# Performance work log

Measured on AMD Instinct MI355X. Metric: run time of the kernel, lower is better.

## Reference

```python
import jax, jax.numpy as jnp
import numpy as np

TOP_K = 2  # num_experts_per_token


def setup_inputs() -> dict:
    key = jax.random.key(0)
    ks = jax.random.split(key, 6)
    B, S, H, F, E = 4, 2048, 1024, 4096, 8  # F = 2 * intermediate_size
    scale = 0.02
    x = jax.random.normal(ks[0], (B, S, H), dtype=jnp.float32)
    gate_w = jax.random.normal(ks[1], (E, H), dtype=jnp.float32) * scale
    w1 = jax.random.normal(ks[2], (E, H, F), dtype=jnp.float32) * scale
    b1 = jnp.zeros((E, F), dtype=jnp.float32)
    w2 = jax.random.normal(ks[3], (E, F, H), dtype=jnp.float32) * scale
    b2 = jnp.zeros((E, H), dtype=jnp.float32)
    return {"x": x, "gate_w": gate_w, "w1": w1, "b1": b1, "w2": w2, "b2": b2}


def reference(x, gate_w, w1, b1, w2, b2):
    # x: [B, S, H]; gate_w: [E, H]; w1: [E, H, F]; b1: [E, F]; w2: [E, F, H]; b2: [E, H]
    E = gate_w.shape[0]
    gate_logits = jnp.einsum('bsh,eh->bse', x, gate_w)
    gate_probs = jax.nn.softmax(gate_logits, axis=-1)
    top_v, top_i = jax.lax.top_k(gate_probs, TOP_K)  # [B, S, K]
    # Combine weight per expert: w[b,s,e] = sum_k top_v[b,s,k] * (top_i[b,s,k] == e)
    onehot = jax.nn.one_hot(top_i, E, dtype=x.dtype)          # [B, S, K, E]
    comb_w = jnp.einsum('bsk,bske->bse', top_v, onehot)       # [B, S, E]
    out = jnp.zeros_like(x)
    for e in range(E):  # small fixed expert loop
        h = jax.nn.silu(jnp.einsum('bsh,hf->bsf', x, w1[e]) + b1[e])
        y = jnp.einsum('bsf,fh->bsh', h, w2[e]) + b2[e]
        out = out + y * comb_w[..., e:e + 1]
    return out
```

## Files before the change

kernel.cpp:

```cpp
#include <hip/hip_runtime.h>
#include <stdint.h>

#define T_TOK 8192
#define HDIM  1024
#define FDIM  4096
#define NEXP  8
#define BT    256
#define RCAP  (2*T_TOK + NEXP*256)
#define LDSB  65536

typedef short  short8  __attribute__((ext_vector_type(8)));
typedef unsigned short ushort8 __attribute__((ext_vector_type(8)));
typedef float  f32x4   __attribute__((ext_vector_type(4)));

#define MFMA __builtin_amdgcn_mfma_f32_16x16x32_bf16

__device__ __forceinline__ unsigned short f2bf(float f) {
  unsigned u = __float_as_uint(f);
  u += 0x7fffu + ((u >> 16) & 1u);
  return (unsigned short)(u >> 16);
}
__device__ __forceinline__ float bf2f(unsigned short u) {
  return __uint_as_float((unsigned)u << 16);
}

__device__ __forceinline__ void gload16(const void* g, void* l) {
  __builtin_amdgcn_global_load_lds(
      (const __attribute__((address_space(1))) void*)g,
      (__attribute__((address_space(3))) void*)l, 16, 0, 0);
}

__global__ __launch_bounds__(256) void k_transp_cvt(const float* __restrict__ in,
                                                    unsigned short* __restrict__ out,
                                                    int K, int N) {
  __shared__ unsigned short s[64][72];
  const float* ine = in + (size_t)blockIdx.z * K * N;
  unsigned short* oute = out + (size_t)blockIdx.z * K * N;
  int k0 = blockIdx.y * 64, n0 = blockIdx.x * 64;
  int t = threadIdx.x;
  int kr = t >> 4, nc = (t & 15) * 4;
#pragma unroll
  for (int it = 0; it < 4; ++it) {
    int k = it * 16 + kr;
    float4 v = *(const float4*)(ine + (size_t)(k0 + k) * N + n0 + nc);
    ushort4 u = make_ushort4(f2bf(v.x), f2bf(v.y), f2bf(v.z), f2bf(v.w));
    *(ushort4*)(&s[k][nc]) = u;
  }
  __syncthreads();
  int nr = t >> 3, kc = (t & 7) * 8;
#pragma unroll
  for (int v = 0; v < 2; ++v) {
    int n = v * 32 + nr;
    ushort8 o;
#pragma unroll
    for (int j = 0; j < 8; ++j) o[j] = s[kc + j][n];
    *(ushort8*)(oute + (size_t)(n0 + n) * K + k0 + kc) = o;
  }
}

__global__ void k_gate(const float* __restrict__ x, const float* __restrict__ gw,
                       unsigned short* __restrict__ xb,
                       int2* __restrict__ eidx, float2* __restrict__ ewt) {
  int tid = threadIdx.x;
  int lane = tid & 63;
  int t = blockIdx.x * 4 + (tid >> 6);
  const float* xr = x + (size_t)t * HDIM;
  unsigned short* xbr = xb + (size_t)t * HDIM;
  float acc[NEXP];
#pragma unroll
  for (int e = 0; e < NEXP; e++) acc[e] = 0.f;
#pragma unroll
  for (int i = 0; i < HDIM / 64; i++) {
    float xv = xr[i * 64 + lane];
    xbr[i * 64 + lane] = f2bf(xv);
#pragma unroll
    for (int e = 0; e < NEXP; e++) acc[e] += xv * gw[e * HDIM + i * 64 + lane];
  }
#pragma unroll
  for (int e = 0; e < NEXP; e++) {
    acc[e] += __shfl_xor(acc[e], 32);
    acc[e] += __shfl_xor(acc[e], 16);
    acc[e] += __shfl_xor(acc[e], 8);
    acc[e] += __shfl_xor(acc[e], 4);
    acc[e] += __shfl_xor(acc[e], 2);
    acc[e] += __shfl_xor(acc[e], 1);
  }
  float m = acc[0];
#pragma unroll
  for (int e = 1; e < NEXP; e++) m = fmaxf(m, acc[e]);
  float p[NEXP]; float s = 0.f;
#pragma unroll
  for (int e = 0; e < NEXP; e++) { p[e] = expf(acc[e] - m); s += p[e]; }
  float inv = 1.f / s;
#pragma unroll
  for (int e = 0; e < NEXP; e++) p[e] *= inv;
  int b0 = 0; float v0 = p[0];
#pragma unroll
  for (int e = 1; e < NEXP; e++) if (p[e] > v0) { v0 = p[e]; b0 = e; }
  int b1i = (b0 == 0) ? 1 : 0; float v1 = p[b1i];
#pragma unroll
  for (int e = 0; e < NEXP; e++) if (e != b0 && p[e] > v1) { v1 = p[e]; b1i = e; }
  if (lane == 0) { eidx[t] = make_int2(b0, b1i); ewt[t] = make_float2(v0, v1); }
}

__global__ void k_compact(const int2* __restrict__ eidx,
                          int* __restrict__ list_tok, int* __restrict__ counts) {
  int e = blockIdx.x;
  int tid = threadIdx.x, lane = tid & 63, wid = tid >> 6;
  __shared__ int sbase;
  __shared__ int wcnt[4];
  if (tid == 0) sbase = 0;
  __syncthreads();
  for (int c = 0; c < T_TOK; c += 256) {
    int t = c + tid;
    int2 ei = eidx[t];
    bool sel = (ei.x == e) || (ei.y == e);
    unsigned long long b = __ballot(sel);
    if (lane == 0) wcnt[wid] = __popcll(b);
    __syncthreads();
    int pre = sbase;
    for (int w = 0; w < wid; w++) pre += wcnt[w];
    int pos = pre + __popcll(b & ((1ull << lane) - 1ull));
    if (sel) list_tok[e * T_TOK + pos] = t;
    __syncthreads();
    if (tid == 0) sbase += wcnt[0] + wcnt[1] + wcnt[2] + wcnt[3];
    __syncthreads();
  }
  if (tid == 0) counts[e] = sbase;
}

__global__ void k_offsets(const int* __restrict__ counts, int* __restrict__ off_pad) {
  if (threadIdx.x == 0) {
    int o = 0;
    off_pad[0] = 0;
    for (int e = 0; e < NEXP; e++) {
      o += ((counts[e] + BT - 1) / BT) * BT;
      off_pad[e + 1] = o;
    }
  }
}

__global__ void k_invert(const int* __restrict__ list_tok, const int* __restrict__ counts,
                         const int* __restrict__ off_pad, const int2* __restrict__ eidx,
                         int2* __restrict__ tok2slot) {
  int e = blockIdx.y;
  int p = blockIdx.x * 256 + threadIdx.x;
  if (p < counts[e]) {
    int t = list_tok[e * T_TOK + p];
    int slot = off_pad[e] + p;
    if (eidx[t].x == e) tok2slot[t].x = slot;
    else                tok2slot[t].y = slot;
  }
}

#define STAGE_A(u_, v_) { \
    char* lb_ = smem + (((v_)&1) ? LDSB : 0) + (u_)*16384; \
    gload16(gA[u_][0] + (size_t)(v_)*128, lb_ + dst0); \
    gload16(gA[u_][1] + (size_t)(v_)*128, lb_ + dst1); }
#define STAGE_B(u_, v_) { \
    char* lb_ = smem + (((v_)&1) ? LDSB : 0) + 32768 + (u_)*16384; \
    gload16(gB[u_][0] + (size_t)(v_)*128, lb_ + dst0); \
    gload16(gB[u_][1] + (size_t)(v_)*128, lb_ + dst1); }

#define PHASE(MA, MB, STAGE_STMT, TAIL_STMT) { \
    short8 aA0 = *(const short8*)(pA0 + (MA)*2048); \
    short8 aA1 = *(const short8*)(pA1 + (MA)*2048); \
    short8 aB0 = *(const short8*)(pA0 + (MB)*2048); \
    short8 aB1 = *(const short8*)(pA1 + (MB)*2048); \
    STAGE_STMT; \
    __builtin_amdgcn_s_barrier(); \
    asm volatile("s_waitcnt lgkmcnt(0)" ::: "memory"); \
    __builtin_amdgcn_sched_barrier(0); \
    __builtin_amdgcn_s_setprio(1); \
    acc[MA][0] = MFMA(aA0, b00, acc[MA][0], 0,0,0); acc[MA][0] = MFMA(aA1, b01, acc[MA][0], 0,0,0); \
    acc[MA][1] = MFMA(aA0, b10, acc[MA][1], 0,0,0); acc[MA][1] = MFMA(aA1, b11, acc[MA][1], 0,0,0); \
    acc[MA][2] = MFMA(aA0, b20, acc[MA][2], 0,0,0); acc[MA][2] = MFMA(aA1, b21, acc[MA][2], 0,0,0); \
    acc[MA][3] = MFMA(aA0, b30, acc[MA][3], 0,0,0); acc[MA][3] = MFMA(aA1, b31, acc[MA][3], 0,0,0); \
    acc[MB][0] = MFMA(aB0, b00, acc[MB][0], 0,0,0); acc[MB][0] = MFMA(aB1, b01, acc[MB][0], 0,0,0); \
    acc[MB][1] = MFMA(aB0, b10, acc[MB][1], 0,0,0); acc[MB][1] = MFMA(aB1, b11, acc[MB][1], 0,0,0); \
    acc[MB][2] = MFMA(aB0, b20, acc[MB][2], 0,0,0); acc[MB][2] = MFMA(aB1, b21, acc[MB][2], 0,0,0); \
    acc[MB][3] = MFMA(aB0, b30, acc[MB][3], 0,0,0); acc[MB][3] = MFMA(aB1, b31, acc[MB][3], 0,0,0); \
    __builtin_amdgcn_s_setprio(0); \
    TAIL_STMT; \
    __builtin_amdgcn_s_barrier(); }

#define READ_B4 \
    short8 b00 = *(const short8*)(pB0),        b01 = *(const short8*)(pB1); \
    short8 b10 = *(const short8*)(pB0 + 2048), b11 = *(const short8*)(pB1 + 2048); \
    short8 b20 = *(const short8*)(pB0 + 4096), b21 = *(const short8*)(pB1 + 4096); \
    short8 b30 = *(const short8*)(pB0 + 6144), b31 = *(const short8*)(pB1 + 6144);

#define GEMM_TILE_LOOP(NT) \
  STAGE_A(0,0); STAGE_A(1,0); STAGE_B(0,0); STAGE_B(1,0); STAGE_B(0,1); STAGE_B(1,1); \
  asm volatile("s_waitcnt vmcnt(4)" ::: "memory"); \
  __builtin_amdgcn_s_barrier(); \
  for (int v = 0; v < (NT); ++v) { \
    const char* bufb = smem + ((v&1) ? LDSB : 0); \
    const char* pA0 = bufb + wm * 16384 + aoff0; \
    const char* pA1 = bufb + wm * 16384 + aoff1; \
    const char* pB0 = bufb + 32768 + (wn >> 1) * 16384 + boff0; \
    const char* pB1 = bufb + 32768 + (wn >> 1) * 16384 + boff1; \
    READ_B4; \
    PHASE(0, 1, { if (v+1 < (NT)) STAGE_A(0, v+1); }, {}); \
    PHASE(2, 3, { if (v+1 < (NT)) STAGE_A(1, v+1); }, {}); \
    PHASE(4, 5, { if (v+2 < (NT)) STAGE_B(0, v+2); }, {}); \
    PHASE(6, 7, { if (v+2 < (NT)) STAGE_B(1, v+2); }, { \
      if (v+2 < (NT))      { asm volatile("s_waitcnt vmcnt(4)" ::: "memory"); } \
      else if (v+1 < (NT)) { asm volatile("s_waitcnt vmcnt(0)" ::: "memory"); } }); \
  }

__global__ __launch_bounds__(512, 2) void k_gemm1(
    const unsigned short* __restrict__ xb, const unsigned short* __restrict__ w1t,
    const float* __restrict__ b1, const int* __restrict__ list_tok,
    const int* __restrict__ counts, const int* __restrict__ off_pad,
    unsigned short* __restrict__ h) {
  extern __shared__ char smem[];
  int wl = (blockIdx.x & 7) * 144 + (blockIdx.x >> 3);
  int r0 = (wl >> 4) * BT;
  int n0 = (wl & 15) * BT;
  if (r0 >= off_pad[NEXP]) return;
  int e = 0;
#pragma unroll
  for (int i = 0; i < NEXP; ++i) if (r0 >= off_pad[i + 1]) e = i + 1;
  int base = off_pad[e], cnt = counts[e];

  int t = threadIdx.x, l = t & 63, w = t >> 6;
  int wm = w >> 2, wn = w & 3;
  int lr = l & 15, g16 = (l >> 4) * 16;
  int swz = (lr & 7) << 4;
  int aoff0 = lr * 128 + (g16 ^ swz);
  int aoff1 = lr * 128 + ((64 + g16) ^ swz);
  int boff0 = (wn & 1) * 8192 + aoff0;
  int boff1 = (wn & 1) * 8192 + aoff1;

  int dst0 = t * 16, dst1 = t * 16 + 8192;
  int srow = t >> 3;
  int skb = (((t & 7) ^ ((t >> 3) & 7)) << 4);
  const char* gA[2][2];
  const char* gB[2][2];
#pragma unroll
  for (int u = 0; u < 2; ++u)
#pragma unroll
    for (int j = 0; j < 2; ++j) {
      int row = u * 128 + srow + 64 * j;
      int se = r0 - base + row;
      int tok = (se < cnt) ? list_tok[e * T_TOK + se] : 0;
      gA[u][j] = (const char*)(xb + (size_t)tok * HDIM) + skb;
      gB[u][j] = (const char*)(w1t + (size_t)e * FDIM * HDIM + (size_t)(n0 + row) * HDIM) + skb;
    }

  f32x4 acc[8][4];
#pragma unroll
  for (int m = 0; m < 8; ++m)
#pragma unroll
    for (int n = 0; n < 4; ++n) acc[m][n] = (f32x4){0.f, 0.f, 0.f, 0.f};

  GEMM_TILE_LOOP(HDIM / 64);

  const float* b1e = b1 + (size_t)e * FDIM + n0;
  unsigned short* Cs = (unsigned short*)smem;
  int lh = l >> 4, lh4 = lh * 4;
  int cswz = lh << 4;
#pragma unroll
  for (int n = 0; n < 4; ++n) {
    int col = wn * 64 + n * 16 + lr;
    int colX = col ^ cswz;
    float bv = b1e[col];
#pragma unroll
    for (int m = 0; m < 8; ++m) {
      int row = wm * 128 + m * 16 + lh4;
#pragma unroll
      for (int i = 0; i < 4; ++i) {
        float vv = acc[m][n][i] + bv;
        float sg = __builtin_amdgcn_rcpf(1.f + __expf(-vv));
        Cs[(size_t)(row + i) * BT + colX] = f2bf(vv * sg);
      }
    }
  }
  __syncthreads();
#pragma unroll
  for (int s = 0; s < 16; ++s) {
    int lin = s * 512 + t;
    int row = lin >> 5, c8 = (lin & 31) * 8;
    int c8X = c8 ^ (((row >> 2) & 3) << 4);
    *(ushort8*)(h + (size_t)(r0 + row) * FDIM + n0 + c8) = *(const ushort8*)(Cs + (size_t)row * BT + c8X);
  }
}

__global__ __launch_bounds__(512, 2) void k_gemm2(
    const unsigned short* __restrict__ h, const unsigned short* __restrict__ w2t,
    const float* __restrict__ b2, const int* __restrict__ off_pad,
    unsigned short* __restrict__ ypartA, unsigned short* __restrict__ ypartB) {
  extern __shared__ char smem[];
  int wl = (blockIdx.x & 7) * 72 + (blockIdx.x >> 3);
  int mB = wl >> 3, rem = wl & 7;
  int r0 = mB * BT;
  int n0 = (rem >> 1) * BT;
  int z  = rem & 1;
  if (r0 >= off_pad[NEXP]) return;
  int e = 0;
#pragma unroll
  for (int i = 0; i < NEXP; ++i) if (r0 >= off_pad[i + 1]) e = i + 1;

  int t = threadIdx.x, l = t & 63, w = t >> 6;
  int wm = w >> 2, wn = w & 3;
  int lr = l & 15, g16 = (l >> 4) * 16;
  int swz = (lr & 7) << 4;
  int aoff0 = lr * 128 + (g16 ^ swz);
  int aoff1 = lr * 128 + ((64 + g16) ^ swz);
  int boff0 = (wn & 1) * 8192 + aoff0;
  int boff1 = (wn & 1) * 8192 + aoff1;

  int dst0 = t * 16, dst1 = t * 16 + 8192;
  int srow = t >> 3;
  int skb = (((t & 7) ^ ((t >> 3) & 7)) << 4);
  const char* gA[2][2];
  const char* gB[2][2];
#pragma unroll
  for (int u = 0; u < 2; ++u)
#pragma unroll
    for (int j = 0; j < 2; ++j) {
      int row = u * 128 + srow + 64 * j;
      gA[u][j] = (const char*)(h + (size_t)(r0 + row) * FDIM + (size_t)z * 2048) + skb;
      gB[u][j] = (const char*)(w2t + (size_t)e * HDIM * FDIM + (size_t)(n0 + row) * FDIM + (size_t)z * 2048) + skb;
    }

  f32x4 acc[8][4];
#pragma unroll
  for (int m = 0; m < 8; ++m)
#pragma unroll
    for (int n = 0; n < 4; ++n) acc[m][n] = (f32x4){0.f, 0.f, 0.f, 0.f};

  GEMM_TILE_LOOP(2048 / 64);

  const float* b2e = b2 + (size_t)e * HDIM + n0;
  unsigned short* yp = z ? ypartB : ypartA;
  unsigned short* Cs = (unsigned short*)smem;
  int lh = l >> 4, lh4 = lh * 4;
  int cswz = lh << 4;
#pragma unroll
  for (int n = 0; n < 4; ++n) {
    int col = wn * 64 + n * 16 + lr;
    int colX = col ^ cswz;
    float bv = (z == 0) ? b2e[col] : 0.f;
#pragma unroll
    for (int m = 0; m < 8; ++m) {
      int row = wm * 128 + m * 16 + lh4;
#pragma unroll
      for (int i = 0; i < 4; ++i)
        Cs[(size_t)(row + i) * BT + colX] = f2bf(acc[m][n][i] + bv);
    }
  }
  __syncthreads();
#pragma unroll
  for (int s = 0; s < 16; ++s) {
    int lin = s * 512 + t;
    int row = lin >> 5, c8 = (lin & 31) * 8;
    int c8X = c8 ^ (((row >> 2) & 3) << 4);
    *(ushort8*)(yp + (size_t)(r0 + row) * HDIM + n0 + c8) = *(const ushort8*)(Cs + (size_t)row * BT + c8X);
  }
}

__global__ void k_reduce(const unsigned short* __restrict__ ypartA,
                         const unsigned short* __restrict__ ypartB,
                         const int2* __restrict__ tok2slot, const float2* __restrict__ ewt,
                         float* __restrict__ out) {
  int idx = blockIdx.x * 256 + threadIdx.x;
  int t = idx >> 7;
  int c8 = (idx & 127) * 8;
  int2 s = tok2slot[t];
  float2 wv = ewt[t];
  ushort8 a0 = *(const ushort8*)(ypartA + (size_t)s.x * HDIM + c8);
  ushort8 a1 = *(const ushort8*)(ypartB + (size_t)s.x * HDIM + c8);
  ushort8 b0 = *(const ushort8*)(ypartA + (size_t)s.y * HDIM + c8);
  ushort8 b1 = *(const ushort8*)(ypartB + (size_t)s.y * HDIM + c8);
  float o[8];
#pragma unroll
  for (int j = 0; j < 8; ++j)
    o[j] = wv.x * (bf2f((unsigned short)a0[j]) + bf2f((unsigned short)a1[j]))
         + wv.y * (bf2f((unsigned short)b0[j]) + bf2f((unsigned short)b1[j]));
  float* op = out + (size_t)t * HDIM + c8;
  *(float4*)op = make_float4(o[0], o[1], o[2], o[3]);
  *(float4*)(op + 4) = make_float4(o[4], o[5], o[6], o[7]);
}

extern "C" void kernel_launch(void* const* d_in, const int* in_sizes, int n_in,
                              void* d_out, int out_size, void* d_ws, size_t ws_size,
                              hipStream_t stream) {
  const float* x  = (const float*)d_in[0];
  const float* gw = (const float*)d_in[1];
  const float* w1 = (const float*)d_in[2];
  const float* b1 = (const float*)d_in[3];
  const float* w2 = (const float*)d_in[4];
  const float* b2 = (const float*)d_in[5];
  float* out = (float*)d_out;

  char* ws = (char*)d_ws;
  size_t off = 0;
  unsigned short* xb = (unsigned short*)(ws + off); off += (size_t)T_TOK * HDIM * 2;
  int2*   eidx = (int2*)(ws + off);   off += (size_t)T_TOK * 8;
  float2* ewt  = (float2*)(ws + off); off += (size_t)T_TOK * 8;
  int2* tok2slot = (int2*)(ws + off); off += (size_t)T_TOK * 8;
  int*  list_tok = (int*)(ws + off);  off += (size_t)NEXP * T_TOK * 4;
  int* counts  = (int*)(ws + off); off += 64;
  int* off_pad = (int*)(ws + off); off += 64;
  off = (off + 255) & ~(size_t)255;
  unsigned short* h      = (unsigned short*)(ws + off); off += (size_t)RCAP * FDIM * 2;
  unsigned short* wT     = (unsigned short*)(ws + off); off += (size_t)NEXP * HDIM * FDIM * 2;
  unsigned short* ypartA = (unsigned short*)(ws + off); off += (size_t)RCAP * HDIM * 2;
  unsigned short* ypartB = (unsigned short*)(ws + off); off += (size_t)RCAP * HDIM * 2;
  if (ws_size < off) return;

  hipFuncSetAttribute((const void*)k_gemm1, hipFuncAttributeMaxDynamicSharedMemorySize, 131072);
  hipFuncSetAttribute((const void*)k_gemm2, hipFuncAttributeMaxDynamicSharedMemorySize, 131072);

  k_gate<<<T_TOK / 4, 256, 0, stream>>>(x, gw, xb, eidx, ewt);
  k_compact<<<NEXP, 256, 0, stream>>>(eidx, list_tok, counts);
  k_offsets<<<1, 64, 0, stream>>>(counts, off_pad);
  k_invert<<<dim3(T_TOK / 256, NEXP), 256, 0, stream>>>(list_tok, counts, off_pad, eidx, tok2slot);
  k_transp_cvt<<<dim3(FDIM / 64, HDIM / 64, NEXP), 256, 0, stream>>>(w1, wT, HDIM, FDIM);
  k_gemm1<<<8 * 144, 512, 131072, stream>>>(xb, wT, b1, list_tok, counts, off_pad, h);
  k_transp_cvt<<<dim3(HDIM / 64, FDIM / 64, NEXP), 256, 0, stream>>>(w2, wT, FDIM, HDIM);
  k_gemm2<<<8 * 72, 512, 131072, stream>>>(h, wT, b2, off_pad, ypartA, ypartB);
  k_reduce<<<T_TOK * (HDIM / 8) / 256, 256, 0, stream>>>(ypartA, ypartB, tok2slot, ewt, out);
}
```

Before: 508.1 us.

## Merge four GEMM pipeline phases into two with reordered independent MFMA chains

The inner GEMM loop goes from four phases to two. Each phase now reads four A fragments, issues two stage loads, and runs 32 MFMAs. The MFMAs are reordered so the low-K and high-K halves of each accumulator are no longer back-to-back, which removes dependent MFMA chains. This halves the barriers per K step and hides MFMA latency better, but it uses more registers for A fragments and coarsens the interleave between global loads and compute.

Result: no change. 512.5 us (+0.9%).

```diff
diff --git a/kernel.cpp b/kernel.cpp
--- a/kernel.cpp
+++ b/kernel.cpp
@@ -162,24 +162,48 @@
     gload16(gB[u_][0] + (size_t)(v_)*128, lb_ + dst0); \
     gload16(gB[u_][1] + (size_t)(v_)*128, lb_ + dst1); }
 
-#define PHASE(MA, MB, STAGE_STMT, TAIL_STMT) { \
-    short8 aA0 = *(const short8*)(pA0 + (MA)*2048); \
-    short8 aA1 = *(const short8*)(pA1 + (MA)*2048); \
-    short8 aB0 = *(const short8*)(pA0 + (MB)*2048); \
-    short8 aB1 = *(const short8*)(pA1 + (MB)*2048); \
+#define PHASE2(M0_, M1_, M2_, M3_, STAGE_STMT, TAIL_STMT) { \
+    short8 a0l = *(const short8*)(pA0 + (M0_)*2048), a0h = *(const short8*)(pA1 + (M0_)*2048); \
+    short8 a1l = *(const short8*)(pA0 + (M1_)*2048), a1h = *(const short8*)(pA1 + (M1_)*2048); \
+    short8 a2l = *(const short8*)(pA0 + (M2_)*2048), a2h = *(const short8*)(pA1 + (M2_)*2048); \
+    short8 a3l = *(const short8*)(pA0 + (M3_)*2048), a3h = *(const short8*)(pA1 + (M3_)*2048); \
     STAGE_STMT; \
     __builtin_amdgcn_s_barrier(); \
     asm volatile("s_waitcnt lgkmcnt(0)" ::: "memory"); \
     __builtin_amdgcn_sched_barrier(0); \
     __builtin_amdgcn_s_setprio(1); \
-    acc[MA][0] = MFMA(aA0, b00, acc[MA][0], 0,0,0); acc[MA][0] = MFMA(aA1, b01, acc[MA][0], 0,0,0); \
-    acc[MA][1] = MFMA(aA0, b10, acc[MA][1], 0,0,0); acc[MA][1] = MFMA(aA1, b11, acc[MA][1], 0,0,0); \
-    acc[MA][2] = MFMA(aA0, b20, acc[MA][2], 0,0,0); acc[MA][2] = MFMA(aA1, b21, acc[MA][2], 0,0,0); \
-    acc[MA][3] = MFMA(aA0, b30, acc[MA][3], 0,0,0); acc[MA][3] = MFMA(aA1, b31, acc[MA][3], 0,0,0); \
-    acc[MB][0] = MFMA(aB0, b00, acc[MB][0], 0,0,0); acc[MB][0] = MFMA(aB1, b01, acc[MB][0], 0,0,0); \
-    acc[MB][1] = MFMA(aB0, b10, acc[MB][1], 0,0,0); acc[MB][1] = MFMA(aB1, b11, acc[MB][1], 0,0,0); \
-    acc[MB][2] = MFMA(aB0, b20, acc[MB][2], 0,0,0); acc[MB][2] = MFMA(aB1, b21, acc[MB][2], 0,0,0); \
-    acc[MB][3] = MFMA(aB0, b30, acc[MB][3], 0,0,0); acc[MB][3] = MFMA(aB1, b31, acc[MB][3], 0,0,0); \
+    acc[M0_][0] = MFMA(a0l, b00, acc[M0_][0], 0,0,0); \
+    acc[M0_][1] = MFMA(a0l, b10, acc[M0_][1], 0,0,0); \
+    acc[M0_][2] = MFMA(a0l, b20, acc[M0_][2], 0,0,0); \
+    acc[M0_][3] = MFMA(a0l, b30, acc[M0_][3], 0,0,0); \
+    acc[M1_][0] = MFMA(a1l, b00, acc[M1_][0], 0,0,0); \
+    acc[M1_][1] = MFMA(a1l, b10, acc[M1_][1], 0,0,0); \
+    acc[M1_][2] = MFMA(a1l, b20, acc[M1_][2], 0,0,0); \
+    acc[M1_][3] = MFMA(a1l, b30, acc[M1_][3], 0,0,0); \
+    acc[M2_][0] = MFMA(a2l, b00, acc[M2_][0], 0,0,0); \
+    acc[M2_][1] = MFMA(a2l, b10, acc[M2_][1], 0,0,0); \
+    acc[M2_][2] = MFMA(a2l, b20, acc[M2_][2], 0,0,0); \
+    acc[M2_][3] = MFMA(a2l, b30, acc[M2_][3], 0,0,0); \
+    acc[M3_][0] = MFMA(a3l, b00, acc[M3_][0], 0,0,0); \
+    acc[M3_][1] = MFMA(a3l, b10, acc[M3_][1], 0,0,0); \
+    acc[M3_][2] = MFMA(a3l, b20, acc[M3_][2], 0,0,0); \
+    acc[M3_][3] = MFMA(a3l, b30, acc[M3_][3], 0,0,0); \
+    acc[M0_][0] = MFMA(a0h, b01, acc[M0_][0], 0,0,0); \
+    acc[M0_][1] = MFMA(a0h, b11, acc[M0_][1], 0,0,0); \
+    acc[M0_][2] = MFMA(a0h, b21, acc[M0_][2], 0,0,0); \
+    acc[M0_][3] = MFMA(a0h, b31, acc[M0_][3], 0,0,0); \
+    acc[M1_][0] = MFMA(a1h, b01, acc[M1_][0], 0,0,0); \
+    acc[M1_][1] = MFMA(a1h, b11, acc[M1_][1], 0,0,0); \
+    acc[M1_][2] = MFMA(a1h, b21, acc[M1_][2], 0,0,0); \
+    acc[M1_][3] = MFMA(a1h, b31, acc[M1_][3], 0,0,0); \
+    acc[M2_][0] = MFMA(a2h, b01, acc[M2_][0], 0,0,0); \
+    acc[M2_][1] = MFMA(a2h, b11, acc[M2_][1], 0,0,0); \
+    acc[M2_][2] = MFMA(a2h, b21, acc[M2_][2], 0,0,0); \
+    acc[M2_][3] = MFMA(a2h, b31, acc[M2_][3], 0,0,0); \
+    acc[M3_][0] = MFMA(a3h, b01, acc[M3_][0], 0,0,0); \
+    acc[M3_][1] = MFMA(a3h, b11, acc[M3_][1], 0,0,0); \
+    acc[M3_][2] = MFMA(a3h, b21, acc[M3_][2], 0,0,0); \
+    acc[M3_][3] = MFMA(a3h, b31, acc[M3_][3], 0,0,0); \
     __builtin_amdgcn_s_setprio(0); \
     TAIL_STMT; \
     __builtin_amdgcn_s_barrier(); }
@@ -201,10 +225,8 @@
     const char* pB0 = bufb + 32768 + (wn >> 1) * 16384 + boff0; \
     const char* pB1 = bufb + 32768 + (wn >> 1) * 16384 + boff1; \
     READ_B4; \
-    PHASE(0, 1, { if (v+1 < (NT)) STAGE_A(0, v+1); }, {}); \
-    PHASE(2, 3, { if (v+1 < (NT)) STAGE_A(1, v+1); }, {}); \
-    PHASE(4, 5, { if (v+2 < (NT)) STAGE_B(0, v+2); }, {}); \
-    PHASE(6, 7, { if (v+2 < (NT)) STAGE_B(1, v+2); }, { \
+    PHASE2(0, 1, 2, 3, { if (v+1 < (NT)) { STAGE_A(0, v+1); STAGE_A(1, v+1); } }, {}); \
+    PHASE2(4, 5, 6, 7, { if (v+2 < (NT)) { STAGE_B(0, v+2); STAGE_B(1, v+2); } }, { \
       if (v+2 < (NT))      { asm volatile("s_waitcnt vmcnt(4)" ::: "memory"); } \
       else if (v+1 < (NT)) { asm volatile("s_waitcnt vmcnt(0)" ::: "memory"); } }); \
   }
```
